# Performance work log

Hardware: AMD Instinct MI355X
Metric: run time of the kernel (lower is better)

## Reference

```python
import jax, jax.numpy as jnp
import numpy as np

B, S, D_IN = 1, 2048, 2048
H, KV, HD = 32, 8, 64          # num_heads, num_kv_groups, head_dim
GS = H // KV                    # group_size
D_OUT = H * HD
EPS = 1e-6


def _rmsnorm(x, w):
    # RMSNormQwen over last dim (head_dim)
    var = jnp.mean(x * x, axis=-1, keepdims=True)
    return x * jax.lax.rsqrt(var + EPS) * w


def _rope(x, cos, sin):
    # rotate-half RoPE; x: [B, heads, S, HD], cos/sin: [S, HD]
    d = x.shape[-1]
    x1, x2 = x[..., : d // 2], x[..., d // 2 :]
    rot = jnp.concatenate([-x2, x1], axis=-1)
    return x * cos + rot * sin


def setup_inputs() -> dict:
    key = jax.random.key(0)
    ks = jax.random.split(key, 8)
    x = jax.random.normal(ks[0], (B, S, D_IN), dtype=jnp.float32)
    Wq = jax.random.normal(ks[1], (D_IN, D_OUT), dtype=jnp.float32) * 0.02
    Wk = jax.random.normal(ks[2], (D_IN, KV * HD), dtype=jnp.float32) * 0.02
    Wv = jax.random.normal(ks[3], (D_IN, KV * HD), dtype=jnp.float32) * 0.02
    Wo = jax.random.normal(ks[4], (D_OUT, D_IN), dtype=jnp.float32) * 0.02
    q_norm_w = jnp.ones((HD,), dtype=jnp.float32)
    k_norm_w = jnp.ones((HD,), dtype=jnp.float32)
    # causal mask: True where masked (j > i)
    mask = jnp.triu(jnp.ones((S, S), dtype=bool), k=1)
    # RoPE tables
    inv_freq = 1.0 / (10000.0 ** (np.arange(0, HD, 2, dtype=np.float32) / HD))
    ang = np.arange(S, dtype=np.float32)[:, None] * inv_freq[None, :]  # [S, HD/2]
    cos = jnp.asarray(np.concatenate([np.cos(ang), np.cos(ang)], axis=-1))
    sin = jnp.asarray(np.concatenate([np.sin(ang), np.sin(ang)], axis=-1))
    return {"x": x, "mask": mask, "cos": cos, "sin": sin,
            "Wq": Wq, "Wk": Wk, "Wv": Wv, "Wo": Wo,
            "q_norm_w": q_norm_w, "k_norm_w": k_norm_w}


def reference(x, mask, cos, sin, Wq, Wk, Wv, Wo, q_norm_w, k_norm_w):
    b, s, _ = x.shape
    q = (x @ Wq).reshape(b, s, H, HD).transpose(0, 2, 1, 3)   # [B,H,S,HD]
    k = (x @ Wk).reshape(b, s, KV, HD).transpose(0, 2, 1, 3)  # [B,KV,S,HD]
    v = (x @ Wv).reshape(b, s, KV, HD).transpose(0, 2, 1, 3)  # [B,KV,S,HD]
    q = _rmsnorm(q, q_norm_w)
    k = _rmsnorm(k, k_norm_w)
    q = _rope(q, cos, sin)
    k = _rope(k, cos, sin)
    # grouped-KV attention without materializing repeated K/V
    qg = q.reshape(b, KV, GS, s, HD)
    scores = jnp.einsum('bkgsd,bktd->bkgst', qg, k)           # [B,KV,GS,S,S]
    scores = jnp.where(mask, -jnp.inf, scores)
    weights = jax.nn.softmax(scores / (HD ** 0.5), axis=-1)
    ctx = jnp.einsum('bkgst,bktd->bkgsd', weights, v)         # [B,KV,GS,S,HD]
    ctx = ctx.reshape(b, H, s, HD).transpose(0, 2, 1, 3).reshape(b, s, D_OUT)
    return ctx @ Wo
```

## Files before the change

### kernel.cpp

```cpp
#include <hip/hip_runtime.h>
#include <hip/hip_bf16.h>
#include <math.h>

#define S_LEN 2048
#define DIN   2048
#define NH    32
#define NKV   8
#define HD    64
#define DOUT  2048
#define QKVN  3072
#define KOFF  2048
#define VOFF  2560

typedef __attribute__((ext_vector_type(8))) short short8v;
typedef __attribute__((ext_vector_type(8))) unsigned short ushort8v;
typedef __attribute__((ext_vector_type(4))) unsigned short ushort4v;
typedef __attribute__((ext_vector_type(4))) float float4v;
typedef __attribute__((ext_vector_type(16))) float float16v;

__device__ __forceinline__ float bf2f(unsigned short u) {
    union { float f; unsigned u; } c; c.u = ((unsigned)u) << 16; return c.f;
}
__device__ __forceinline__ unsigned short f2bf(float f) {
    union { float f; unsigned u; } c; c.f = f;
    unsigned r = c.u + 0x7fffu + ((c.u >> 16) & 1u);
    return (unsigned short)(r >> 16);
}
__device__ __forceinline__ unsigned short f2h(float f) {
    union { _Float16 h; unsigned short u; } c; c.h = (_Float16)f; return c.u;
}
__device__ __forceinline__ float h2f(unsigned short u) {
    union { _Float16 h; unsigned short u; } c; c.u = u; return (float)c.h;
}
__device__ __forceinline__ unsigned cvtpk(float lo, float hi) {
    unsigned r;
    asm("v_cvt_pk_bf16_f32 %0, %1, %2" : "=v"(r) : "v"(lo), "v"(hi));
    return r;
}

__global__ __launch_bounds__(256) void prep(const float* __restrict__ Wq,
                                            const float* __restrict__ Wk,
                                            const float* __restrict__ Wv,
                                            const float* __restrict__ Wo,
                                            const float* __restrict__ x,
                                            unsigned short* __restrict__ W1,
                                            unsigned short* __restrict__ WoT,
                                            unsigned short* __restrict__ XB) {
    __shared__ float t[32][33];
    const int a = blockIdx.x;
    const int tx = threadIdx.x & 31, ty = threadIdx.x >> 5;
    if (a < 6144) {
        const int n0 = (a % 96) * 32, k0 = (a / 96) * 32;
        const float* src; int nn0, Nsrc;
        if (n0 < KOFF)      { src = Wq; nn0 = n0;        Nsrc = DOUT; }
        else if (n0 < VOFF) { src = Wk; nn0 = n0 - KOFF; Nsrc = 512; }
        else                { src = Wv; nn0 = n0 - VOFF; Nsrc = 512; }
#pragma unroll
        for (int j = ty; j < 32; j += 8)
            t[j][tx] = src[(size_t)(k0 + j) * Nsrc + nn0 + tx];
        __syncthreads();
#pragma unroll
        for (int j = ty; j < 32; j += 8)
            W1[(size_t)(n0 + j) * DIN + k0 + tx] = f2bf(t[tx][j]);
    } else if (a < 10240) {
        const int b = a - 6144;
        const int n0 = (b % 64) * 32, k0 = (b / 64) * 32;
#pragma unroll
        for (int j = ty; j < 32; j += 8)
            t[j][tx] = Wo[(size_t)(k0 + j) * DIN + n0 + tx];
        __syncthreads();
#pragma unroll
        for (int j = ty; j < 32; j += 8)
            WoT[(size_t)(n0 + j) * DOUT + k0 + tx] = f2bf(t[tx][j]);
    } else {
        const int i = (a - 10240) * 1024 + threadIdx.x * 4;
        float4 v = *(const float4*)(x + i);
        XB[i + 0] = f2bf(v.x); XB[i + 1] = f2bf(v.y);
        XB[i + 2] = f2bf(v.z); XB[i + 3] = f2bf(v.w);
    }
}

template <int FUSE>
__global__ __launch_bounds__(256) void gemm64(const unsigned short* __restrict__ A,
                                              const unsigned short* __restrict__ Bt,
                                              void* __restrict__ Cv, int M, int N, int K,
                                              const float* __restrict__ qnw,
                                              const float* __restrict__ knw,
                                              const float* __restrict__ cosb,
                                              const float* __restrict__ sinb) {
    __shared__ __attribute__((aligned(16))) unsigned short As[2 * 128 * 64];
    __shared__ __attribute__((aligned(16))) unsigned short Bs[2 * 64 * 64];
    const int tid = threadIdx.x, lane = tid & 63, w = tid >> 6;
    const int bm = blockIdx.y * 128, bn = blockIdx.x * 64;
    const int wm = w * 32;

    float4v acc[2][4];
#pragma unroll
    for (int i = 0; i < 2; i++)
#pragma unroll
        for (int j = 0; j < 4; j++) acc[i][j] = (float4v){0.f, 0.f, 0.f, 0.f};

    const int srow = lane >> 3;
    const int schk = (lane & 7) ^ srow;
    const unsigned short* Ag[4];
    const unsigned short* Bg[2];
#pragma unroll
    for (int g = 0; g < 4; g++)
        Ag[g] = A + (size_t)(bm + w * 32 + g * 8 + srow) * K + schk * 8;
#pragma unroll
    for (int g = 0; g < 2; g++)
        Bg[g] = Bt + (size_t)(bn + w * 16 + g * 8 + srow) * K + schk * 8;

    auto STAGE = [&](int t, int b) {
        const size_t ko = (size_t)t * 64;
        unsigned short* Ad = As + b * (128 * 64) + (w * 32) * 64;
        unsigned short* Bd = Bs + b * (64 * 64) + (w * 16) * 64;
#pragma unroll
        for (int g = 0; g < 4; g++)
            __builtin_amdgcn_global_load_lds(
                (const __attribute__((address_space(1))) void*)(Ag[g] + ko),
                (__attribute__((address_space(3))) void*)(Ad + g * 8 * 64), 16, 0, 0);
#pragma unroll
        for (int g = 0; g < 2; g++)
            __builtin_amdgcn_global_load_lds(
                (const __attribute__((address_space(1))) void*)(Bg[g] + ko),
                (__attribute__((address_space(3))) void*)(Bd + g * 8 * 64), 16, 0, 0);
    };

    const int frow = lane & 15, quad = lane >> 4, sw = frow & 7;
    const int NT = K >> 6;

    STAGE(0, 0);

    for (int t = 0; t < NT; t++) {
        const int c = t & 1;
        if (t + 1 < NT) {
            STAGE(t + 1, c ^ 1);
            asm volatile("s_waitcnt vmcnt(6)" ::: "memory");
        } else {
            asm volatile("s_waitcnt vmcnt(0)" ::: "memory");
        }
        __builtin_amdgcn_s_barrier();
        __builtin_amdgcn_sched_barrier(0);

        const unsigned short* Ab = As + c * (128 * 64);
        const unsigned short* Bb = Bs + c * (64 * 64);
        short8v af[2][2], bf[4][2];
#pragma unroll
        for (int fm = 0; fm < 2; fm++)
#pragma unroll
            for (int ks = 0; ks < 2; ks++)
                af[fm][ks] = *(const short8v*)(Ab + (wm + fm * 16 + frow) * 64 +
                                               (((ks * 4 + quad) ^ sw) * 8));
#pragma unroll
        for (int fn = 0; fn < 4; fn++)
#pragma unroll
            for (int ks = 0; ks < 2; ks++)
                bf[fn][ks] = *(const short8v*)(Bb + (fn * 16 + frow) * 64 +
                                               (((ks * 4 + quad) ^ sw) * 8));
        __builtin_amdgcn_s_setprio(1);
#pragma unroll
        for (int ks = 0; ks < 2; ks++)
#pragma unroll
            for (int fm = 0; fm < 2; fm++)
#pragma unroll
                for (int fn = 0; fn < 4; fn++)
                    acc[fm][fn] = __builtin_amdgcn_mfma_f32_16x16x32_bf16(
                        af[fm][ks], bf[fn][ks], acc[fm][fn], 0, 0, 0);
        __builtin_amdgcn_s_setprio(0);

        if (t + 1 < NT) {
            asm volatile("s_waitcnt lgkmcnt(0)" ::: "memory");
            __builtin_amdgcn_sched_barrier(0);
            __builtin_amdgcn_s_barrier();
        }
    }

    const int quad4 = lane >> 4, col16 = lane & 15;
    if constexpr (FUSE == 1) {
        unsigned short* C = (unsigned short*)Cv;
        const int head = bn >> 6;
        if (head < 40) {
            const float* nw = (head < 32) ? qnw : knw;
            float wv[4];
#pragma unroll
            for (int fn = 0; fn < 4; fn++) wv[fn] = nw[fn * 16 + col16];
#pragma unroll
            for (int fm = 0; fm < 2; fm++)
#pragma unroll
                for (int r = 0; r < 4; r++) {
                    float x0 = acc[fm][0][r], x1 = acc[fm][1][r];
                    float x2 = acc[fm][2][r], x3 = acc[fm][3][r];
                    float ss = x0 * x0 + x1 * x1 + x2 * x2 + x3 * x3;
                    ss += __shfl_xor(ss, 1); ss += __shfl_xor(ss, 2);
                    ss += __shfl_xor(ss, 4); ss += __shfl_xor(ss, 8);
                    const float inv = rsqrtf(ss * (1.0f / 64.0f) + 1e-6f);
                    float xn[4] = {x0 * inv * wv[0], x1 * inv * wv[1],
                                   x2 * inv * wv[2], x3 * inv * wv[3]};
                    const int row = bm + wm + fm * 16 + quad4 * 4 + r;
                    const float* cr = cosb + (size_t)row * HD;
                    const float* sr = sinb + (size_t)row * HD;
#pragma unroll
                    for (int fn = 0; fn < 4; fn++) {
                        const float rot = (fn < 2) ? -xn[fn + 2] : xn[fn - 2];
                        const float res = xn[fn] * cr[fn * 16 + col16] +
                                          rot * sr[fn * 16 + col16];
                        C[(size_t)row * N + bn + fn * 16 + col16] = f2bf(res);
                    }
                }
        } else {
#pragma unroll
            for (int fm = 0; fm < 2; fm++)
#pragma unroll
                for (int fn = 0; fn < 4; fn++)
#pragma unroll
                    for (int r = 0; r < 4; r++)
                        C[(size_t)(bm + wm + fm * 16 + quad4 * 4 + r) * N +
                          bn + fn * 16 + col16] = f2bf(acc[fm][fn][r]);
        }
    } else {
        float* C = (float*)Cv;
#pragma unroll
        for (int fm = 0; fm < 2; fm++)
#pragma unroll
            for (int fn = 0; fn < 4; fn++)
#pragma unroll
                for (int r = 0; r < 4; r++)
                    C[(size_t)(bm + wm + fm * 16 + quad4 * 4 + r) * N +
                      bn + fn * 16 + col16] = acc[fm][fn][r];
    }
}

#define KSTR 88

__global__ __launch_bounds__(256) void flash_part(const unsigned short* __restrict__ qb,
                                                  const unsigned short* __restrict__ kb,
                                                  const unsigned short* __restrict__ vb,
                                                  unsigned short* __restrict__ Op,
                                                  float* __restrict__ Lp) {
    __shared__ __attribute__((aligned(16))) unsigned short Ks[64 * KSTR];
    __shared__ __attribute__((aligned(16))) unsigned short Vt[64 * KSTR];

    const int tid = threadIdx.x, lane = tid & 63, w = tid >> 6;
    const int sl = lane & 31, hi = lane >> 5, hi8 = hi * 8;
    const int bid = blockIdx.x;
    const int g = bid & 7;
    const int p = (bid >> 3) & 31;
    const int s = bid >> 8;
    const int h = g * 4 + w;

    const int s0a = p * 32, s0b = (63 - p) * 32;
    const int nta = (s0a + 95) >> 6;
    const int nA  = s ? 0 : nta;
    const int bLo = s ? (17 - nta) : 0;
    const int nB  = s ? 16 : (17 - nta);
    const int nT  = nA + nB;

    const float C1 = 0.18033688011112042f;
    const float C2 = 12.262908856239697f;

    unsigned short* Oh = Op + (size_t)s * S_LEN * DOUT;
    float* Lh = Lp + (size_t)s * S_LEN * NH;

    int s0 = nA ? s0a : s0b;

    short8v qf[4];
#pragma unroll
    for (int ksq = 0; ksq < 4; ksq++)
        qf[ksq] = *(const short8v*)(qb + (size_t)(s0 + sl) * QKVN + h * HD +
                                    ksq * 16 + hi8);

    float16v O[2];
#pragma unroll
    for (int df = 0; df < 2; df++)
#pragma unroll
        for (int r = 0; r < 16; r++) O[df][r] = 0.f;
    float lsum = 0.f;

    const int kkey = tid >> 2, kch = tid & 3;
    const unsigned short* kg = kb + (size_t)kkey * QKVN + g * HD + kch * 16;
    const int vkey = tid & 63, vdb = tid >> 6;
    const unsigned short* vg = vb + (size_t)vkey * QKVN + g * HD + vdb * 16;

    auto epi = [&](int sbase) {
        float lt = lsum + __shfl_xor(lsum, 32);
        if (hi == 0) Lh[(size_t)(sbase + sl) * NH + h] = lt;
#pragma unroll
        for (int df = 0; df < 2; df++)
#pragma unroll
            for (int r = 0; r < 16; r++) {
                const int row = sbase + (r & 3) + 8 * (r >> 2) + 4 * hi;
                Oh[(size_t)row * DOUT + h * HD + df * 32 + sl] = f2h(O[df][r]);
            }
    };

    const int it0 = nA ? 0 : bLo;
    const size_t p0 = (size_t)it0 * 64 * QKVN;
    ushort8v ka0 = *(const ushort8v*)(kg + p0);
    ushort8v ka1 = *(const ushort8v*)(kg + p0 + 8);
    ushort8v va0 = *(const ushort8v*)(vg + p0);
    ushort8v va1 = *(const ushort8v*)(vg + p0 + 8);

    for (int j = 0; j < nT; j++) {
        if (j > 0) __syncthreads();
        {
            unsigned short* kd = Ks + kkey * KSTR + kch * 16;
            *(ushort8v*)kd = ka0;
            *(ushort8v*)(kd + 8) = ka1;
            unsigned short* vd = Vt + (size_t)(vdb * 16) * KSTR + vkey;
#pragma unroll
            for (int jj = 0; jj < 8; jj++) vd[jj * KSTR] = va0[jj];
#pragma unroll
            for (int jj = 0; jj < 8; jj++) vd[(8 + jj) * KSTR] = va1[jj];
        }
        __syncthreads();
        if (j + 1 < nT) {
            const int itn = (j + 1 < nA) ? (j + 1) : (bLo + (j + 1 - nA));
            const size_t off = (size_t)itn * 64 * QKVN;
            ka0 = *(const ushort8v*)(kg + off);
            ka1 = *(const ushort8v*)(kg + off + 8);
            va0 = *(const ushort8v*)(vg + off);
            va1 = *(const ushort8v*)(vg + off + 8);
        }
        if (nA && j == nA) {
            epi(s0a);
#pragma unroll
            for (int df = 0; df < 2; df++)
#pragma unroll
                for (int r = 0; r < 16; r++) O[df][r] = 0.f;
            lsum = 0.f;
            s0 = s0b;
#pragma unroll
            for (int ksq = 0; ksq < 4; ksq++)
                qf[ksq] = *(const short8v*)(qb + (size_t)(s0b + sl) * QKVN +
                                            h * HD + ksq * 16 + hi8);
        }

        const int it = (j < nA) ? j : (bLo + (j - nA));
        const int t0 = it * 64;
        const bool edge = (t0 + 63 > s0);

#pragma unroll
        for (int b = 0; b < 2; b++) {
            short8v kf[4];
#pragma unroll
            for (int ksq = 0; ksq < 4; ksq++)
                kf[ksq] = *(const short8v*)(Ks + (32 * b + sl) * KSTR +
                                            ksq * 16 + hi8);
            float16v sct;
#pragma unroll
            for (int r = 0; r < 16; r++) sct[r] = 0.f;
#pragma unroll
            for (int ksq = 0; ksq < 4; ksq++)
                sct = __builtin_amdgcn_mfma_f32_32x32x16_bf16(kf[ksq], qf[ksq],
                                                              sct, 0, 0, 0);
#pragma unroll
            for (int r = 0; r < 16; r++) {
                float arg = sct[r] * C1 - C2;
                if (edge) {
                    const int kglob = t0 + 32 * b + (r & 3) + 8 * (r >> 2) + 4 * hi;
                    arg = (kglob <= s0 + sl) ? arg : -100.f;
                }
                const float pv = exp2f(arg);
                sct[r] = pv;
                lsum += pv;
            }
            unsigned pk[8];
#pragma unroll
            for (int i = 0; i < 8; i++) pk[i] = cvtpk(sct[2 * i], sct[2 * i + 1]);
#pragma unroll
            for (int kk = 0; kk < 2; kk++) {
                const unsigned x0 = pk[4 * kk + 0], x1 = pk[4 * kk + 1];
                const unsigned y0 = pk[4 * kk + 2], y1 = pk[4 * kk + 3];
                const unsigned a0 = __shfl_xor(x0, 32), a1 = __shfl_xor(x1, 32);
                const unsigned b0 = __shfl_xor(y0, 32), b1 = __shfl_xor(y1, 32);
                union { unsigned u[4]; short8v v; } pa;
                pa.u[0] = hi ? b0 : x0;
                pa.u[1] = hi ? b1 : x1;
                pa.u[2] = hi ? y0 : a0;
                pa.u[3] = hi ? y1 : a1;
                const int ks = 2 * b + kk;
#pragma unroll
                for (int df = 0; df < 2; df++) {
                    const short8v vf = *(const short8v*)(Vt + (size_t)(df * 32 + sl) * KSTR +
                                                         ks * 16 + hi8);
                    O[df] = __builtin_amdgcn_mfma_f32_32x32x16_bf16(pa.v, vf,
                                                                    O[df], 0, 0, 0);
                }
            }
        }
    }

    epi(s0);
}

__global__ __launch_bounds__(256) void combine(unsigned short* O01,
                                               const float* __restrict__ Lp) {
    const int i4 = (blockIdx.x * 256 + threadIdx.x) * 4;
    const int srow = i4 >> 11, hh = (i4 & 2047) >> 6;
    float l = Lp[(size_t)srow * NH + hh];
    ushort4v o0 = *(const ushort4v*)(O01 + i4);
    float acc[4];
#pragma unroll
    for (int j = 0; j < 4; j++) acc[j] = h2f(o0[j]);
    if (srow >= 1024) {
        l += Lp[(size_t)S_LEN * NH + (size_t)srow * NH + hh];
        ushort4v o1 = *(const ushort4v*)(O01 + (size_t)S_LEN * DOUT + i4);
#pragma unroll
        for (int j = 0; j < 4; j++) acc[j] += h2f(o1[j]);
    }
    const float inv = 1.0f / l;
    ushort4v r;
#pragma unroll
    for (int j = 0; j < 4; j++) r[j] = f2bf(acc[j] * inv);
    *(ushort4v*)(O01 + i4) = r;
}

extern "C" void kernel_launch(void* const* d_in, const int* in_sizes, int n_in,
                              void* d_out, int out_size, void* d_ws, size_t ws_size,
                              hipStream_t stream) {
    const float* x    = (const float*)d_in[0];
    const float* cosb = (const float*)d_in[2];
    const float* sinb = (const float*)d_in[3];
    const float* Wq   = (const float*)d_in[4];
    const float* Wk   = (const float*)d_in[5];
    const float* Wv   = (const float*)d_in[6];
    const float* Wo   = (const float*)d_in[7];
    const float* qw   = (const float*)d_in[8];
    const float* kw   = (const float*)d_in[9];
    float* out = (float*)d_out;

    unsigned short* W1  = (unsigned short*)d_ws;
    unsigned short* XB  = W1 + (size_t)QKVN * DIN;
    unsigned short* WoT = XB + (size_t)S_LEN * DIN;
    unsigned short* QKV = WoT + (size_t)DIN * DOUT;
    unsigned short* Op  = (unsigned short*)d_ws;
    float*          Lp  = (float*)(Op + (size_t)2 * S_LEN * DOUT);
    unsigned short* CTX = Op;

    dim3 blk256(256);

    prep<<<dim3(14336), blk256, 0, stream>>>(Wq, Wk, Wv, Wo, x, W1, WoT, XB);

    gemm64<1><<<dim3(QKVN / 64, S_LEN / 128), blk256, 0, stream>>>(
        XB, W1, QKV, S_LEN, QKVN, DIN, qw, kw, cosb, sinb);

    flash_part<<<dim3(NKV * 32 * 2), blk256, 0, stream>>>(
        QKV, QKV + KOFF, QKV + VOFF, Op, Lp);

    combine<<<dim3(S_LEN * DOUT / 1024), blk256, 0, stream>>>(Op, Lp);

    gemm64<0><<<dim3(DIN / 64, S_LEN / 128), blk256, 0, stream>>>(
        CTX, WoT, out, S_LEN, DIN, DOUT, nullptr, nullptr, nullptr, nullptr);
}
```

Measured before the change: 236.6 us.

## Double-buffer K/V shared tiles in flash attention with two-stage prefetch

The flash attention kernel now keeps two LDS buffers for K and transposed V. The next tile is committed while the current one is computed, so only one barrier is needed per iteration, and global loads run two tiles ahead. The V transpose now pairs two keys per thread with byte permutes, giving 32-bit LDS stores instead of 16-bit scalar stores. The second query block is also preloaded up front, and MFMA sections are wrapped in s_setprio. In exchange, the kernel doubles LDS use and adds register pressure, which may lower occupancy.

```diff
diff --git a/kernel.cpp b/kernel.cpp
--- a/kernel.cpp
+++ b/kernel.cpp
@@ -238,8 +238,8 @@
                                                   const unsigned short* __restrict__ vb,
                                                   unsigned short* __restrict__ Op,
                                                   float* __restrict__ Lp) {
-    __shared__ __attribute__((aligned(16))) unsigned short Ks[64 * KSTR];
-    __shared__ __attribute__((aligned(16))) unsigned short Vt[64 * KSTR];
+    __shared__ __attribute__((aligned(16))) unsigned short Ks[2][64 * KSTR];
+    __shared__ __attribute__((aligned(16))) unsigned short Vt[2][64 * KSTR];
 
     const int tid = threadIdx.x, lane = tid & 63, w = tid >> 6;
     const int sl = lane & 31, hi = lane >> 5, hi8 = hi * 8;
@@ -264,11 +264,17 @@
 
     int s0 = nA ? s0a : s0b;
 
-    short8v qf[4];
+    short8v qf[4], qfB[4];
 #pragma unroll
     for (int ksq = 0; ksq < 4; ksq++)
         qf[ksq] = *(const short8v*)(qb + (size_t)(s0 + sl) * QKVN + h * HD +
                                     ksq * 16 + hi8);
+    if (nA) {
+#pragma unroll
+        for (int ksq = 0; ksq < 4; ksq++)
+            qfB[ksq] = *(const short8v*)(qb + (size_t)(s0b + sl) * QKVN + h * HD +
+                                         ksq * 16 + hi8);
+    }
 
     float16v O[2];
 #pragma unroll
@@ -279,8 +285,9 @@
 
     const int kkey = tid >> 2, kch = tid & 3;
     const unsigned short* kg = kb + (size_t)kkey * QKVN + g * HD + kch * 16;
-    const int vkey = tid & 63, vdb = tid >> 6;
-    const unsigned short* vg = vb + (size_t)vkey * QKVN + g * HD + vdb * 16;
+    const int kp = tid & 31, vdbb = tid >> 5;
+    const unsigned short* vg0 = vb + (size_t)(2 * kp) * QKVN + g * HD + vdbb * 8;
+    const unsigned short* vg1 = vg0 + QKVN;
 
     auto epi = [&](int sbase) {
         float lt = lsum + __shfl_xor(lsum, 32);
@@ -294,34 +301,40 @@
             }
     };
 
-    const int it0 = nA ? 0 : bLo;
-    const size_t p0 = (size_t)it0 * 64 * QKVN;
-    ushort8v ka0 = *(const ushort8v*)(kg + p0);
-    ushort8v ka1 = *(const ushort8v*)(kg + p0 + 8);
-    ushort8v va0 = *(const ushort8v*)(vg + p0);
-    ushort8v va1 = *(const ushort8v*)(vg + p0 + 8);
+    auto tileIdx = [&](int j) { return (j < nA) ? j : (bLo + (j - nA)); };
+
+    ushort8v ka0, ka1, va0, va1;
+    auto LOADREGS = [&](int it) {
+        const size_t off = (size_t)it * 64 * QKVN;
+        ka0 = *(const ushort8v*)(kg + off);
+        ka1 = *(const ushort8v*)(kg + off + 8);
+        va0 = *(const ushort8v*)(vg0 + off);
+        va1 = *(const ushort8v*)(vg1 + off);
+    };
+    auto COMMIT = [&](int b) {
+        unsigned short* kd = Ks[b] + kkey * KSTR + kch * 16;
+        *(ushort8v*)kd = ka0;
+        *(ushort8v*)(kd + 8) = ka1;
+        union { ushort8v v; unsigned d[4]; } ua, ub;
+        ua.v = va0; ub.v = va1;
+        unsigned short* vd = Vt[b] + (size_t)(vdbb * 8) * KSTR + 2 * kp;
+#pragma unroll
+        for (int i = 0; i < 8; i++) {
+            const unsigned sel = (i & 1) ? 0x07060302u : 0x05040100u;
+            const unsigned word = __builtin_amdgcn_perm(ub.d[i >> 1], ua.d[i >> 1], sel);
+            *(unsigned*)(vd + (size_t)i * KSTR) = word;
+        }
+    };
+
+    LOADREGS(tileIdx(0));
+    COMMIT(0);
+    if (nT > 1) LOADREGS(tileIdx(1));
 
     for (int j = 0; j < nT; j++) {
-        if (j > 0) __syncthreads();
-        {
-            unsigned short* kd = Ks + kkey * KSTR + kch * 16;
-            *(ushort8v*)kd = ka0;
-            *(ushort8v*)(kd + 8) = ka1;
-            unsigned short* vd = Vt + (size_t)(vdb * 16) * KSTR + vkey;
-#pragma unroll
-            for (int jj = 0; jj < 8; jj++) vd[jj * KSTR] = va0[jj];
-#pragma unroll
-            for (int jj = 0; jj < 8; jj++) vd[(8 + jj) * KSTR] = va1[jj];
-        }
+        const int cur = j & 1;
         __syncthreads();
-        if (j + 1 < nT) {
-            const int itn = (j + 1 < nA) ? (j + 1) : (bLo + (j + 1 - nA));
-            const size_t off = (size_t)itn * 64 * QKVN;
-            ka0 = *(const ushort8v*)(kg + off);
-            ka1 = *(const ushort8v*)(kg + off + 8);
-            va0 = *(const ushort8v*)(vg + off);
-            va1 = *(const ushort8v*)(vg + off + 8);
-        }
+        if (j + 1 < nT) COMMIT(cur ^ 1);
+        if (j + 2 < nT) LOADREGS(tileIdx(j + 2));
         if (nA && j == nA) {
             epi(s0a);
 #pragma unroll
@@ -331,13 +344,10 @@
             lsum = 0.f;
             s0 = s0b;
 #pragma unroll
-            for (int ksq = 0; ksq < 4; ksq++)
-                qf[ksq] = *(const short8v*)(qb + (size_t)(s0b + sl) * QKVN +
-                                            h * HD + ksq * 16 + hi8);
-        }
-
-        const int it = (j < nA) ? j : (bLo + (j - nA));
-        const int t0 = it * 64;
+            for (int ksq = 0; ksq < 4; ksq++) qf[ksq] = qfB[ksq];
+        }
+
+        const int t0 = tileIdx(j) * 64;
         const bool edge = (t0 + 63 > s0);
 
 #pragma unroll
@@ -345,15 +355,17 @@
             short8v kf[4];
 #pragma unroll
             for (int ksq = 0; ksq < 4; ksq++)
-                kf[ksq] = *(const short8v*)(Ks + (32 * b + sl) * KSTR +
+                kf[ksq] = *(const short8v*)(Ks[cur] + (32 * b + sl) * KSTR +
                                             ksq * 16 + hi8);
             float16v sct;
 #pragma unroll
             for (int r = 0; r < 16; r++) sct[r] = 0.f;
+            __builtin_amdgcn_s_setprio(1);
 #pragma unroll
             for (int ksq = 0; ksq < 4; ksq++)
                 sct = __builtin_amdgcn_mfma_f32_32x32x16_bf16(kf[ksq], qf[ksq],
                                                               sct, 0, 0, 0);
+            __builtin_amdgcn_s_setprio(0);
 #pragma unroll
             for (int r = 0; r < 16; r++) {
                 float arg = sct[r] * C1 - C2;
@@ -380,13 +392,16 @@
                 pa.u[2] = hi ? y0 : a0;
                 pa.u[3] = hi ? y1 : a1;
                 const int ks = 2 * b + kk;
+                __builtin_amdgcn_s_setprio(1);
 #pragma unroll
                 for (int df = 0; df < 2; df++) {
-                    const short8v vf = *(const short8v*)(Vt + (size_t)(df * 32 + sl) * KSTR +
+                    const short8v vf = *(const short8v*)(Vt[cur] +
+                                                         (size_t)(df * 32 + sl) * KSTR +
                                                          ks * 16 + hi8);
                     O[df] = __builtin_amdgcn_mfma_f32_32x32x16_bf16(pa.v, vf,
                                                                     O[df], 0, 0, 0);
                 }
+                __builtin_amdgcn_s_setprio(0);
             }
         }
     }
```

Result: no change. 236.6 us (-0.0%).
